# Optimization experiments

Hardware: AMD Instinct MI355X
Metric: run time of the kernel (lower is better)

## Reference

```python
import jax, jax.numpy as jnp
import numpy as np
import math

B, L, DV = 8, 2048, 512
FACTOR = 5
SAMPLE_K = min(FACTOR * int(np.ceil(np.log(L))), L)  # 40
N_TOP = min(FACTOR * int(np.ceil(np.log(L))), L)     # 40


def setup_inputs() -> dict:
    key = jax.random.key(0)
    k1, k2, k3, k4, k5 = jax.random.split(key, 5)
    x = jax.random.normal(k1, (B, L, DV), dtype=jnp.float32)
    Wq = jax.random.normal(k2, (DV, DV), dtype=jnp.float32) * (1.0 / math.sqrt(DV))
    Wk = jax.random.normal(k3, (DV, DV), dtype=jnp.float32) * (1.0 / math.sqrt(DV))
    Wv = jax.random.normal(k4, (DV, DV), dtype=jnp.float32) * (1.0 / math.sqrt(DV))
    index_sample = jax.random.randint(k5, (L, SAMPLE_K), 0, L, dtype=jnp.int32)
    return {"x": x, "Wq": Wq, "Wk": Wk, "Wv": Wv, "index_sample": index_sample}


def reference(x, Wq, Wk, Wv, index_sample):
    # Projections (torch Linear, no bias): y = x @ W.T
    Q = x @ Wq.T  # [B, L, D]
    K = x @ Wk.T  # [B, L, D]
    V = x @ Wv.T  # [B, L, D]
    b, L_Q, D = Q.shape
    L_K = K.shape[1]

    # _prob_QK: sample keys per query, score sparsity measure M
    K_sample = K[:, index_sample, :]                       # [B, L_Q, sample_k, D]
    QK_sample = jnp.einsum('bld,blsd->bls', Q, K_sample)   # [B, L_Q, sample_k]
    M = QK_sample.max(axis=-1) - QK_sample.sum(axis=-1) / L_K  # [B, L_Q]
    _, M_top = jax.lax.top_k(M, N_TOP)                     # [B, n_top]

    Q_reduce = jnp.take_along_axis(Q, M_top[:, :, None], axis=1)  # [B, n_top, D]
    scores = jnp.einsum('bud,bkd->buk', Q_reduce, K)       # [B, n_top, L_K]
    scores = scores * (1.0 / math.sqrt(D))

    # mask_flag=False -> initial context is mean of V broadcast over queries
    attn = jax.nn.softmax(scores, axis=-1)
    context = jnp.broadcast_to(V.mean(axis=1, keepdims=True), (b, L_Q, D))
    upd = attn @ V                                         # [B, n_top, D]
    context = context.at[jnp.arange(b)[:, None], M_top].set(upd)
    return context
```

## Files before the change

kernel.cpp:

```cpp
#include <hip/hip_runtime.h>
#include <hip/hip_bf16.h>
#include <hip/hip_fp16.h>
#include <math.h>

#define BATCH 8
#define LSEQ 2048
#define DIM 512
#define SK 40
#define NTOP 40

typedef __attribute__((ext_vector_type(8))) short bf16x8;
typedef __attribute__((ext_vector_type(4))) float f32x4;

__device__ inline void split1(float f, ushort& h, ushort& l) {
    __hip_bfloat16 bh = __float2bfloat16(f);
    float r = f - __bfloat162float(bh);
    __hip_bfloat16 bl = __float2bfloat16(r);
    h = *reinterpret_cast<ushort*>(&bh);
    l = *reinterpret_cast<ushort*>(&bl);
}

__global__ __launch_bounds__(256) void convert_all(
    const float* __restrict__ x,
    const float* __restrict__ w0, const float* __restrict__ w1, const float* __restrict__ w2,
    ushort* __restrict__ xh, ushort* __restrict__ xl,
    ushort* __restrict__ wh, ushort* __restrict__ wl)
{
    const int bx = blockIdx.x;
    const float* src;
    ushort *dh, *dl;
    int i;
    if (bx < 8192) {
        i = (bx * 256 + (int)threadIdx.x) * 4;
        src = x; dh = xh; dl = xl;
    } else {
        const int j = bx - 8192;
        const int z = j >> 8;
        src = (z == 0) ? w0 : (z == 1) ? w1 : w2;
        dh = wh + (size_t)z * DIM * DIM;
        dl = wl + (size_t)z * DIM * DIM;
        i = ((j & 255) * 256 + (int)threadIdx.x) * 4;
    }
    float4 v = *reinterpret_cast<const float4*>(src + i);
    ushort4 h, l;
    split1(v.x, h.x, l.x); split1(v.y, h.y, l.y);
    split1(v.z, h.z, l.z); split1(v.w, h.w, l.w);
    *reinterpret_cast<ushort4*>(dh + i) = h;
    *reinterpret_cast<ushort4*>(dl + i) = l;
}

__device__ inline void load_lds16(const void* g, void* l) {
    __builtin_amdgcn_global_load_lds(
        (const __attribute__((address_space(1))) void*)g,
        (__attribute__((address_space(3))) void*)l, 16, 0, 0);
}

__global__ __launch_bounds__(256) void gemm_mfma(
    const ushort* __restrict__ xh, const ushort* __restrict__ xl,
    const ushort* __restrict__ whAll, const ushort* __restrict__ wlAll,
    float* __restrict__ Q, float* __restrict__ K, float* __restrict__ V,
    ushort* __restrict__ Khalf)
{
    const ushort* Wh = whAll + (size_t)blockIdx.z * DIM * DIM;
    const ushort* Wl = wlAll + (size_t)blockIdx.z * DIM * DIM;
    float* C = (blockIdx.z == 0) ? Q : (blockIdx.z == 1) ? K : V;
    const bool wk = (Khalf != nullptr) && (blockIdx.z == 1);

    __shared__ ushort Ah[128 * 32], Al[128 * 32], Bh[128 * 32], Bl[128 * 32];

    const int tid  = threadIdx.x;
    const int lane = tid & 63;
    const int w    = tid >> 6;
    const int row0 = blockIdx.x * 128;
    const int col0 = blockIdx.y * 128;
    const int wr = w >> 1, wc = w & 1;

    const int rA  = w * 16 + (lane >> 2);
    const int sh_ = (lane & 3) ^ ((rA >> 1) & 3);
    const size_t aoff = (size_t)(row0 + rA) * DIM + sh_ * 8;
    const size_t boff = (size_t)(col0 + rA) * DIM + sh_ * 8;

    f32x4 acc[4][4];
    #pragma unroll
    for (int i = 0; i < 4; ++i)
        #pragma unroll
        for (int j = 0; j < 4; ++j)
            acc[i][j] = (f32x4){0.f, 0.f, 0.f, 0.f};

    const int rbA = wr * 64 + (lane & 15);
    const int rbB = wc * 64 + (lane & 15);
    const int kh  = lane >> 4;

    for (int k0 = 0; k0 < DIM; k0 += 32) {
        load_lds16(xh + aoff + k0,            &Ah[w * 512]);
        load_lds16(xh + aoff + 64 * DIM + k0, &Ah[2048 + w * 512]);
        load_lds16(xl + aoff + k0,            &Al[w * 512]);
        load_lds16(xl + aoff + 64 * DIM + k0, &Al[2048 + w * 512]);
        load_lds16(Wh + boff + k0,            &Bh[w * 512]);
        load_lds16(Wh + boff + 64 * DIM + k0, &Bh[2048 + w * 512]);
        load_lds16(Wl + boff + k0,            &Bl[w * 512]);
        load_lds16(Wl + boff + 64 * DIM + k0, &Bl[2048 + w * 512]);
        __syncthreads();

        bf16x8 fah[4], fal[4], fbh[4], fbl[4];
        #pragma unroll
        for (int mf = 0; mf < 4; ++mf) {
            const int r = rbA + mf * 16;
            const int off = r * 32 + (kh ^ ((r >> 1) & 3)) * 8;
            fah[mf] = *reinterpret_cast<const bf16x8*>(&Ah[off]);
            fal[mf] = *reinterpret_cast<const bf16x8*>(&Al[off]);
        }
        #pragma unroll
        for (int nf = 0; nf < 4; ++nf) {
            const int r = rbB + nf * 16;
            const int off = r * 32 + (kh ^ ((r >> 1) & 3)) * 8;
            fbh[nf] = *reinterpret_cast<const bf16x8*>(&Bh[off]);
            fbl[nf] = *reinterpret_cast<const bf16x8*>(&Bl[off]);
        }
        #pragma unroll
        for (int mf = 0; mf < 4; ++mf)
            #pragma unroll
            for (int nf = 0; nf < 4; ++nf) {
                acc[mf][nf] = __builtin_amdgcn_mfma_f32_16x16x32_bf16(fah[mf], fbh[nf], acc[mf][nf], 0, 0, 0);
                acc[mf][nf] = __builtin_amdgcn_mfma_f32_16x16x32_bf16(fal[mf], fbh[nf], acc[mf][nf], 0, 0, 0);
                acc[mf][nf] = __builtin_amdgcn_mfma_f32_16x16x32_bf16(fah[mf], fbl[nf], acc[mf][nf], 0, 0, 0);
            }
        __syncthreads();
    }

    #pragma unroll
    for (int mf = 0; mf < 4; ++mf)
        #pragma unroll
        for (int nf = 0; nf < 4; ++nf) {
            const size_t rbase = (size_t)(row0 + wr * 64 + mf * 16 + (lane >> 4) * 4);
            const int    cidx  = col0 + wc * 64 + nf * 16 + (lane & 15);
            float* cp = C + rbase * DIM + cidx;
            #pragma unroll
            for (int j = 0; j < 4; ++j) {
                cp[(size_t)j * DIM] = acc[mf][nf][j];
                if (wk) {
                    __half h = __float2half(acc[mf][nf][j]);
                    Khalf[(rbase + j) * DIM + cidx] = *reinterpret_cast<ushort*>(&h);
                }
            }
        }
}

#define BM 64
#define BN 64
#define BKD 32
__global__ __launch_bounds__(256) void gemm_qkv(
    const float* __restrict__ x,
    const float* __restrict__ Wq, const float* __restrict__ Wk, const float* __restrict__ Wv,
    float* __restrict__ Q, float* __restrict__ K, float* __restrict__ V)
{
    const float* W;
    float* C;
    if (blockIdx.z == 0)      { W = Wq; C = Q; }
    else if (blockIdx.z == 1) { W = Wk; C = K; }
    else                      { W = Wv; C = V; }

    __shared__ float As[BKD][BM];
    __shared__ float Bs[BKD][BN];

    const int tid  = threadIdx.x;
    const int row0 = blockIdx.x * BM;
    const int col0 = blockIdx.y * BN;
    const int ty   = tid >> 4;
    const int tx   = tid & 15;
    const int lrow = tid >> 3;
    const int lkq  = tid & 7;

    float acc[4][4] = {};
    for (int k0 = 0; k0 < DIM; k0 += BKD) {
        #pragma unroll
        for (int h = 0; h < 2; ++h) {
            const int arow = lrow + h * 32;
            float4 va = *reinterpret_cast<const float4*>(&x[(size_t)(row0 + arow) * DIM + k0 + lkq * 4]);
            As[lkq * 4 + 0][arow] = va.x; As[lkq * 4 + 1][arow] = va.y;
            As[lkq * 4 + 2][arow] = va.z; As[lkq * 4 + 3][arow] = va.w;
            float4 vb = *reinterpret_cast<const float4*>(&W[(size_t)(col0 + arow) * DIM + k0 + lkq * 4]);
            Bs[lkq * 4 + 0][arow] = vb.x; Bs[lkq * 4 + 1][arow] = vb.y;
            Bs[lkq * 4 + 2][arow] = vb.z; Bs[lkq * 4 + 3][arow] = vb.w;
        }
        __syncthreads();
        #pragma unroll
        for (int kk = 0; kk < BKD; ++kk) {
            float4 a4 = *reinterpret_cast<const float4*>(&As[kk][ty * 4]);
            float4 b4 = *reinterpret_cast<const float4*>(&Bs[kk][tx * 4]);
            float af[4] = {a4.x, a4.y, a4.z, a4.w};
            float bf[4] = {b4.x, b4.y, b4.z, b4.w};
            #pragma unroll
            for (int i = 0; i < 4; ++i)
                #pragma unroll
                for (int j = 0; j < 4; ++j)
                    acc[i][j] += af[i] * bf[j];
        }
        __syncthreads();
    }
    #pragma unroll
    for (int i = 0; i < 4; ++i) {
        float4 o = make_float4(acc[i][0], acc[i][1], acc[i][2], acc[i][3]);
        *reinterpret_cast<float4*>(&C[(size_t)(row0 + ty * 4 + i) * DIM + col0 + tx * 4]) = o;
    }
}

__global__ __launch_bounds__(512) void m_and_vp(
    const float* __restrict__ Q, const float* __restrict__ K,
    const ushort* __restrict__ Khalf,
    const float* __restrict__ V, const int* __restrict__ smp,
    float* __restrict__ M, float* __restrict__ P)
{
    const int bid = blockIdx.x;
    if (bid < 2048) {
        const int wv   = threadIdx.x >> 6;
        const int lane = threadIdx.x & 63;
        const int b    = bid & 7;
        const int l    = (bid >> 3) * 8 + wv;

        const float* qr = Q + ((size_t)b * LSEQ + l) * DIM;
        float4 q0 = *reinterpret_cast<const float4*>(&qr[lane * 8]);
        float4 q1 = *reinterpret_cast<const float4*>(&qr[lane * 8 + 4]);
        const float qf[8] = {q0.x, q0.y, q0.z, q0.w, q1.x, q1.y, q1.z, q1.w};

        const int* sp = smp + l * SK;
        float mx = -1e30f, sm = 0.0f;

        if (Khalf) {
            const ushort* Kb = Khalf + (size_t)b * LSEQ * DIM;
            for (int s = 0; s < SK; s += 8) {
                int4 i0 = *reinterpret_cast<const int4*>(sp + s);
                int4 i1 = *reinterpret_cast<const int4*>(sp + s + 4);
                const int id[8] = {i0.x, i0.y, i0.z, i0.w, i1.x, i1.y, i1.z, i1.w};
                float p[8];
                #pragma unroll
                for (int j = 0; j < 8; ++j) {
                    float4 hv = *reinterpret_cast<const float4*>(Kb + (size_t)id[j] * DIM + lane * 8);
                    const __half* h = reinterpret_cast<const __half*>(&hv);
                    float d = 0.0f;
                    #pragma unroll
                    for (int e = 0; e < 8; ++e) d = fmaf(qf[e], __half2float(h[e]), d);
                    p[j] = d;
                }
                #pragma unroll
                for (int o = 32; o; o >>= 1) {
                    #pragma unroll
                    for (int j = 0; j < 8; ++j) p[j] += __shfl_xor(p[j], o, 64);
                }
                #pragma unroll
                for (int j = 0; j < 8; ++j) { mx = fmaxf(mx, p[j]); sm += p[j]; }
            }
        } else {
            const float* Kb = K + (size_t)b * LSEQ * DIM;
            for (int s = 0; s < SK; s += 8) {
                int4 i0 = *reinterpret_cast<const int4*>(sp + s);
                int4 i1 = *reinterpret_cast<const int4*>(sp + s + 4);
                const int id[8] = {i0.x, i0.y, i0.z, i0.w, i1.x, i1.y, i1.z, i1.w};
                float p[8];
                #pragma unroll
                for (int j = 0; j < 8; ++j) {
                    const float* r = Kb + (size_t)id[j] * DIM + lane * 8;
                    float4 u0 = *reinterpret_cast<const float4*>(r);
                    float4 u1 = *reinterpret_cast<const float4*>(r + 4);
                    p[j] = q0.x*u0.x + q0.y*u0.y + q0.z*u0.z + q0.w*u0.w
                         + q1.x*u1.x + q1.y*u1.y + q1.z*u1.z + q1.w*u1.w;
                }
                #pragma unroll
                for (int o = 32; o; o >>= 1) {
                    #pragma unroll
                    for (int j = 0; j < 8; ++j) p[j] += __shfl_xor(p[j], o, 64);
                }
                #pragma unroll
                for (int j = 0; j < 8; ++j) { mx = fmaxf(mx, p[j]); sm += p[j]; }
            }
        }
        if (lane == 0) M[(size_t)b * LSEQ + l] = mx - sm * (1.0f / LSEQ);
    } else {
        const int j = bid - 2048;
        const int b = j & 7, c = j >> 3;
        const int d = threadIdx.x;
        const float* vp = V + ((size_t)b * LSEQ + c * 128) * DIM + d;
        float s = 0.0f;
        for (int r = 0; r < 128; ++r) s += vp[(size_t)r * DIM];
        P[(size_t)(b * 16 + c) * DIM + d] = s;
    }
}

__global__ __launch_bounds__(512) void refine_kernel(
    const float* __restrict__ Mc, const float* __restrict__ Q,
    const float* __restrict__ K, const int* __restrict__ smp,
    float* __restrict__ Mf)
{
    const int b   = blockIdx.x & 7;
    const int lch = blockIdx.x >> 3;
    const int wv   = threadIdx.x >> 6;
    const int lane = threadIdx.x & 63;
    __shared__ float sT0;

    if (threadIdx.x < 64) {
        float v[32];
        #pragma unroll
        for (int r = 0; r < 32; ++r) v[r] = Mc[(size_t)b * LSEQ + lane + r * 64];
        float T0 = -1e30f;
        for (int t = 0; t < 56; ++t) {
            float bv = -1e30f; int bk = 0;
            #pragma unroll
            for (int r = 0; r < 32; ++r) if (v[r] > bv) { bv = v[r]; bk = r; }
            int bl = lane;
            #pragma unroll
            for (int o = 32; o; o >>= 1) {
                float ov = __shfl_xor(bv, o, 64);
                int   obl = __shfl_xor(bl, o, 64);
                int   obk = __shfl_xor(bk, o, 64);
                if (ov > bv || (ov == bv && obl < bl)) { bv = ov; bl = obl; bk = obk; }
            }
            if (lane == bl) v[bk] = -1e30f;
            T0 = bv;
        }
        if (lane == 0) sT0 = T0;
    }
    __syncthreads();
    const float thr = sT0 - 0.25f;

    const int lbase = lch * 64 + wv * 8;
    for (int i = 0; i < 8; ++i) {
        const int l = lbase + i;
        const float cheap = Mc[(size_t)b * LSEQ + l];
        if (cheap > thr) {
            const float* qr = Q + ((size_t)b * LSEQ + l) * DIM;
            float4 q0 = *reinterpret_cast<const float4*>(&qr[lane * 8]);
            float4 q1 = *reinterpret_cast<const float4*>(&qr[lane * 8 + 4]);
            const int* sp = smp + l * SK;
            const float* Kb = K + (size_t)b * LSEQ * DIM;
            float mx = -1e30f, sm = 0.0f;
            for (int s = 0; s < SK; s += 8) {
                int4 i0 = *reinterpret_cast<const int4*>(sp + s);
                int4 i1 = *reinterpret_cast<const int4*>(sp + s + 4);
                const int id[8] = {i0.x, i0.y, i0.z, i0.w, i1.x, i1.y, i1.z, i1.w};
                float p[8];
                #pragma unroll
                for (int j = 0; j < 8; ++j) {
                    const float* r = Kb + (size_t)id[j] * DIM + lane * 8;
                    float4 u0 = *reinterpret_cast<const float4*>(r);
                    float4 u1 = *reinterpret_cast<const float4*>(r + 4);
                    p[j] = q0.x*u0.x + q0.y*u0.y + q0.z*u0.z + q0.w*u0.w
                         + q1.x*u1.x + q1.y*u1.y + q1.z*u1.z + q1.w*u1.w;
                }
                #pragma unroll
                for (int o = 32; o; o >>= 1) {
                    #pragma unroll
                    for (int j = 0; j < 8; ++j) p[j] += __shfl_xor(p[j], o, 64);
                }
                #pragma unroll
                for (int j = 0; j < 8; ++j) { mx = fmaxf(mx, p[j]); sm += p[j]; }
            }
            if (lane == 0) Mf[(size_t)b * LSEQ + l] = mx - sm * (1.0f / LSEQ);
        } else {
            if (lane == 0) Mf[(size_t)b * LSEQ + l] = cheap;
        }
    }
}

__global__ __launch_bounds__(512) void topk_vr(
    const float* __restrict__ M, const float* __restrict__ P,
    int* __restrict__ topidx, float* __restrict__ vmean)
{
    if (blockIdx.x < 8) {
        if (threadIdx.x >= 64) return;
        const int b = blockIdx.x;
        const int lane = threadIdx.x;
        float v[32];
        #pragma unroll
        for (int r = 0; r < 32; ++r) v[r] = M[(size_t)b * LSEQ + lane + r * 64];
        for (int t = 0; t < NTOP; ++t) {
            float bv = -1e30f; int bk = 0;
            #pragma unroll
            for (int r = 0; r < 32; ++r) if (v[r] > bv) { bv = v[r]; bk = r; }
            int bi = lane + bk * 64;
            #pragma unroll
            for (int o = 32; o; o >>= 1) {
                float ov = __shfl_xor(bv, o, 64);
                int   oi = __shfl_xor(bi, o, 64);
                if (ov > bv || (ov == bv && oi < bi)) { bv = ov; bi = oi; }
            }
            if (lane == (bi & 63)) v[bi >> 6] = -1e30f;
            if (lane == 0) topidx[b * NTOP + t] = bi;
        }
    } else {
        const int b = blockIdx.x - 8;
        const int d = threadIdx.x;
        float s = 0.0f;
        #pragma unroll
        for (int c = 0; c < 16; ++c) s += P[(size_t)(b * 16 + c) * DIM + d];
        vmean[b * DIM + d] = s * (1.0f / LSEQ);
    }
}

__global__ __launch_bounds__(256) void fill_out(
    const float4* __restrict__ vmean4, float4* __restrict__ out4)
{
    const int f = blockIdx.x * 256 + threadIdx.x;
    const int d4 = f & 127;
    const int b  = f >> 18;
    out4[f] = vmean4[b * 128 + d4];
}

__global__ __launch_bounds__(256) void scores_kernel(
    const float* __restrict__ Q, const float* __restrict__ K,
    const int* __restrict__ topidx, float* __restrict__ S)
{
    const int b  = blockIdx.x & 7;
    const int lc = blockIdx.x >> 3;
    __shared__ float Qs[40 * 132];
    __shared__ float Ks[64 * 132];
    __shared__ int tix[NTOP];
    const int tid = threadIdx.x;
    const int lt  = tid & 31;
    const int ug  = tid >> 5;
    float acc[2][5] = {};

    if (tid < NTOP) tix[tid] = topidx[b * NTOP + tid];
    __syncthreads();

    for (int d0 = 0; d0 < DIM; d0 += 128) {
        for (int j = tid; j < 1280; j += 256) {
            const int u = j >> 5, d4 = j & 31;
            *reinterpret_cast<float4*>(&Qs[u * 132 + d4 * 4]) =
                *reinterpret_cast<const float4*>(&Q[((size_t)b * LSEQ + tix[u]) * DIM + d0 + d4 * 4]);
        }
        for (int j = tid; j < 2048; j += 256) {
            const int l = j >> 5, d4 = j & 31;
            *reinterpret_cast<float4*>(&Ks[l * 132 + d4 * 4]) =
                *reinterpret_cast<const float4*>(&K[((size_t)b * LSEQ + lc * 64 + l) * DIM + d0 + d4 * 4]);
        }
        __syncthreads();
        for (int d4 = 0; d4 < 32; ++d4) {
            float4 ka = *reinterpret_cast<const float4*>(&Ks[lt * 132 + d4 * 4]);
            float4 kb = *reinterpret_cast<const float4*>(&Ks[(lt + 32) * 132 + d4 * 4]);
            #pragma unroll
            for (int i = 0; i < 5; ++i) {
                float4 q = *reinterpret_cast<const float4*>(&Qs[(ug + i * 8) * 132 + d4 * 4]);
                acc[0][i] += q.x * ka.x + q.y * ka.y + q.z * ka.z + q.w * ka.w;
                acc[1][i] += q.x * kb.x + q.y * kb.y + q.z * kb.z + q.w * kb.w;
            }
        }
        __syncthreads();
    }
    const float scale = 0.044194173824159216f;
    #pragma unroll
    for (int i = 0; i < 5; ++i) {
        const int u = ug + i * 8;
        S[((size_t)(b * NTOP + u)) * LSEQ + lc * 64 + lt]      = acc[0][i] * scale;
        S[((size_t)(b * NTOP + u)) * LSEQ + lc * 64 + lt + 32] = acc[1][i] * scale;
    }
}

__global__ __launch_bounds__(256) void softmax_kernel(
    const float* __restrict__ S, float* __restrict__ Pt)
{
    const int row = blockIdx.x;
    const int b = row / NTOP, u = row % NTOP;
    __shared__ float red[4];
    const int tid  = threadIdx.x;
    const int lane = tid & 63;
    const int wave = tid >> 6;
    const float* sr = S + (size_t)row * LSEQ;

    float v[8];
    float mx = -1e30f;
    #pragma unroll
    for (int j = 0; j < 8; ++j) { v[j] = sr[tid + j * 256]; mx = fmaxf(mx, v[j]); }
    #pragma unroll
    for (int o = 32; o; o >>= 1) mx = fmaxf(mx, __shfl_xor(mx, o, 64));
    if (lane == 0) red[wave] = mx;
    __syncthreads();
    mx = fmaxf(fmaxf(red[0], red[1]), fmaxf(red[2], red[3]));
    __syncthreads();

    float s = 0.0f;
    #pragma unroll
    for (int j = 0; j < 8; ++j) { v[j] = __expf(v[j] - mx); s += v[j]; }
    #pragma unroll
    for (int o = 32; o; o >>= 1) s += __shfl_xor(s, o, 64);
    if (lane == 0) red[wave] = s;
    __syncthreads();
    const float rec = 1.0f / (red[0] + red[1] + red[2] + red[3]);

    #pragma unroll
    for (int j = 0; j < 8; ++j)
        Pt[((size_t)b * LSEQ + tid + j * 256) * NTOP + u] = v[j] * rec;
}

__global__ __launch_bounds__(512) void pv_partial(
    const float* __restrict__ Pt, const float* __restrict__ V, float* __restrict__ Ppart)
{
    const int b  = blockIdx.x & 7;
    const int lc = blockIdx.x >> 3;
    const int d  = threadIdx.x;
    float part[NTOP] = {};
    for (int lg = 0; lg < 32; ++lg) {
        const int l = lc * 128 + lg * 4;
        const float v0 = V[((size_t)b * LSEQ + l + 0) * DIM + d];
        const float v1 = V[((size_t)b * LSEQ + l + 1) * DIM + d];
        const float v2 = V[((size_t)b * LSEQ + l + 2) * DIM + d];
        const float v3 = V[((size_t)b * LSEQ + l + 3) * DIM + d];
        const float4* p0 = reinterpret_cast<const float4*>(Pt + ((size_t)b * LSEQ + l + 0) * NTOP);
        const float4* p1 = reinterpret_cast<const float4*>(Pt + ((size_t)b * LSEQ + l + 1) * NTOP);
        const float4* p2 = reinterpret_cast<const float4*>(Pt + ((size_t)b * LSEQ + l + 2) * NTOP);
        const float4* p3 = reinterpret_cast<const float4*>(Pt + ((size_t)b * LSEQ + l + 3) * NTOP);
        #pragma unroll
        for (int u4 = 0; u4 < 10; ++u4) {
            float4 a = p0[u4], bb = p1[u4], c = p2[u4], dd = p3[u4];
            part[u4*4+0] = fmaf(a.x, v0, fmaf(bb.x, v1, fmaf(c.x, v2, fmaf(dd.x, v3, part[u4*4+0]))));
            part[u4*4+1] = fmaf(a.y, v0, fmaf(bb.y, v1, fmaf(c.y, v2, fmaf(dd.y, v3, part[u4*4+1]))));
            part[u4*4+2] = fmaf(a.z, v0, fmaf(bb.z, v1, fmaf(c.z, v2, fmaf(dd.z, v3, part[u4*4+2]))));
            part[u4*4+3] = fmaf(a.w, v0, fmaf(bb.w, v1, fmaf(c.w, v2, fmaf(dd.w, v3, part[u4*4+3]))));
        }
    }
    #pragma unroll
    for (int u = 0; u < NTOP; ++u)
        Ppart[(((size_t)(b * 16 + lc)) * NTOP + u) * DIM + d] = part[u];
}

__global__ __launch_bounds__(512) void pv_reduce(
    const float* __restrict__ Ppart, const int* __restrict__ topidx, float* __restrict__ out)
{
    const int row = blockIdx.x;
    const int b = row / NTOP, u = row % NTOP;
    const int d = threadIdx.x;
    float s = 0.0f;
    #pragma unroll
    for (int lc = 0; lc < 16; ++lc)
        s += Ppart[(((size_t)(b * 16 + lc)) * NTOP + u) * DIM + d];
    out[((size_t)b * LSEQ + topidx[row]) * DIM + d] = s;
}

__global__ __launch_bounds__(256) void att_kernel(
    const float* __restrict__ Q, const float* __restrict__ K, const float* __restrict__ V,
    const int* __restrict__ topidx, float* __restrict__ out)
{
    const int b = blockIdx.x / NTOP;
    const int u = blockIdx.x % NTOP;
    const int l0 = topidx[b * NTOP + u];

    __shared__ float p[LSEQ];
    __shared__ float redm[4];
    __shared__ float reds[4];

    const int tid  = threadIdx.x;
    const int lane = tid & 63;
    const int wave = tid >> 6;

    const float* qr = Q + ((size_t)b * LSEQ + l0) * DIM;
    float4 q0 = *reinterpret_cast<const float4*>(&qr[lane * 8]);
    float4 q1 = *reinterpret_cast<const float4*>(&qr[lane * 8 + 4]);
    const float scale = 0.044194173824159216f;

    for (int it = 0; it < 512; ++it) {
        const int l = wave * 512 + it;
        const float* kr = K + ((size_t)b * LSEQ + l) * DIM;
        float4 k0 = *reinterpret_cast<const float4*>(&kr[lane * 8]);
        float4 k1 = *reinterpret_cast<const float4*>(&kr[lane * 8 + 4]);
        float d = q0.x * k0.x + q0.y * k0.y + q0.z * k0.z + q0.w * k0.w
                + q1.x * k1.x + q1.y * k1.y + q1.z * k1.z + q1.w * k1.w;
        #pragma unroll
        for (int o = 32; o; o >>= 1) d += __shfl_xor(d, o, 64);
        if (lane == 0) p[l] = d * scale;
    }
    __syncthreads();

    float mx = -1e30f;
    for (int i = tid; i < LSEQ; i += 256) mx = fmaxf(mx, p[i]);
    #pragma unroll
    for (int o = 32; o; o >>= 1) mx = fmaxf(mx, __shfl_xor(mx, o, 64));
    if (lane == 0) redm[wave] = mx;
    __syncthreads();
    mx = fmaxf(fmaxf(redm[0], redm[1]), fmaxf(redm[2], redm[3]));

    float s = 0.0f;
    for (int i = tid; i < LSEQ; i += 256) {
        float e = __expf(p[i] - mx);
        s += e;
        p[i] = e;
    }
    #pragma unroll
    for (int o = 32; o; o >>= 1) s += __shfl_xor(s, o, 64);
    if (lane == 0) reds[wave] = s;
    __syncthreads();
    const float rec = 1.0f / (reds[0] + reds[1] + reds[2] + reds[3]);

    float s0 = 0.0f, s1 = 0.0f;
    const float* vp = V + (size_t)b * LSEQ * DIM;
    for (int l = 0; l < LSEQ; ++l) {
        const float w = p[l];
        s0 += w * vp[(size_t)l * DIM + tid];
        s1 += w * vp[(size_t)l * DIM + tid + 256];
    }
    float* orow = out + ((size_t)b * LSEQ + l0) * DIM;
    orow[tid]       = s0 * rec;
    orow[tid + 256] = s1 * rec;
}

extern "C" void kernel_launch(void* const* d_in, const int* in_sizes, int n_in,
                              void* d_out, int out_size, void* d_ws, size_t ws_size,
                              hipStream_t stream)
{
    const float* x   = (const float*)d_in[0];
    const float* Wq  = (const float*)d_in[1];
    const float* Wk  = (const float*)d_in[2];
    const float* Wv  = (const float*)d_in[3];
    const int*   smp = (const int*)d_in[4];
    float* out = (float*)d_out;

    const size_t NQKV = (size_t)BATCH * LSEQ * DIM;
    float* ws = (float*)d_ws;

    float* Q     = ws;
    float* K     = Q + NQKV;
    float* V     = K + NQKV;
    float* Mb    = V + NQKV;
    float* vmP   = Mb + BATCH * LSEQ;
    float* vmean = vmP + BATCH * 16 * DIM;
    float* S     = vmean + BATCH * DIM;
    float* Pt    = S + (size_t)BATCH * NTOP * LSEQ;
    float* Mf    = Pt + (size_t)BATCH * NTOP * LSEQ;
    float* Ppart = Mf + (size_t)BATCH * LSEQ;
    int*   topidx = (int*)(Ppart + (size_t)BATCH * 16 * NTOP * DIM);
    ushort* xh = (ushort*)(topidx + BATCH * NTOP);
    ushort* xl = xh + NQKV;
    ushort* wh = xl + NQKV;
    ushort* wl = wh + (size_t)3 * DIM * DIM;
    ushort* Khalf = wl + (size_t)3 * DIM * DIM;
    const size_t need_fast2 = (size_t)((char*)(Khalf + NQKV) - (char*)d_ws);
    const size_t need_fast  = (size_t)((char*)Khalf - (char*)d_ws);
    const size_t need_mid   = (size_t)((char*)(topidx + BATCH * NTOP) - (char*)d_ws);

    const bool fast2 = ws_size >= need_fast2;
    const bool fast  = ws_size >= need_fast;
    const bool mid   = ws_size >= need_mid;

    if (mid) {
        ushort* kh = nullptr;
        if (fast) {
            kh = fast2 ? Khalf : nullptr;
            convert_all<<<8960, 256, 0, stream>>>(x, Wq, Wk, Wv, xh, xl, wh, wl);
            gemm_mfma<<<dim3(BATCH * LSEQ / 128, DIM / 128, 3), 256, 0, stream>>>(
                xh, xl, wh, wl, Q, K, V, kh);
        } else {
            gemm_qkv<<<dim3(BATCH * LSEQ / BM, DIM / BN, 3), 256, 0, stream>>>(
                x, Wq, Wk, Wv, Q, K, V);
        }
        m_and_vp<<<2176, 512, 0, stream>>>(Q, K, kh, V, smp, Mb, vmP);
        const float* Msel = Mb;
        if (kh) {
            refine_kernel<<<256, 512, 0, stream>>>(Mb, Q, K, smp, Mf);
            Msel = Mf;
        }
        topk_vr<<<16, 512, 0, stream>>>(Msel, vmP, topidx, vmean);
        fill_out<<<(BATCH * LSEQ * DIM / 4) / 256, 256, 0, stream>>>(
            (const float4*)vmean, (float4*)out);
        scores_kernel<<<256, 256, 0, stream>>>(Q, K, topidx, S);
        softmax_kernel<<<BATCH * NTOP, 256, 0, stream>>>(S, Pt);
        pv_partial<<<128, 512, 0, stream>>>(Pt, V, Ppart);
        pv_reduce<<<BATCH * NTOP, 512, 0, stream>>>(Ppart, topidx, out);
    } else {
        float* Qf = ws;
        float* Kf = Qf + NQKV;
        float* Vf = Kf + NQKV;
        float* Mfb = Vf + NQKV;
        int*   ti = (int*)(Mfb + (size_t)BATCH * LSEQ);
        float* Pf = (float*)(ti + BATCH * NTOP);
        float* vm = Pf + (size_t)BATCH * 16 * DIM;

        gemm_qkv<<<dim3(BATCH * LSEQ / BM, DIM / BN, 3), 256, 0, stream>>>(
            x, Wq, Wk, Wv, Qf, Kf, Vf);
        m_and_vp<<<2176, 512, 0, stream>>>(Qf, Kf, nullptr, Vf, smp, Mfb, Pf);
        topk_vr<<<16, 512, 0, stream>>>(Mfb, Pf, ti, vm);
        fill_out<<<(BATCH * LSEQ * DIM / 4) / 256, 256, 0, stream>>>(
            (const float4*)vm, (float4*)out);
        att_kernel<<<BATCH * NTOP, 256, 0, stream>>>(Qf, Kf, Vf, ti, out);
    }
}
```

Baseline: 373.7 us.

## Fuse candidate refinement into top-k kernel and move fp16 K conversion to own kernel

```diff
diff --git a/kernel.cpp b/kernel.cpp
--- a/kernel.cpp
+++ b/kernel.cpp
@@ -8,8 +8,10 @@
 #define DIM 512
 #define SK 40
 #define NTOP 40
+#define NCAND 56
 
 typedef __attribute__((ext_vector_type(8))) short bf16x8;
+typedef __attribute__((ext_vector_type(8))) ushort u16x8;
 typedef __attribute__((ext_vector_type(4))) float f32x4;
 
 __device__ inline void split1(float f, ushort& h, ushort& l) {
@@ -58,13 +60,11 @@
 __global__ __launch_bounds__(256) void gemm_mfma(
     const ushort* __restrict__ xh, const ushort* __restrict__ xl,
     const ushort* __restrict__ whAll, const ushort* __restrict__ wlAll,
-    float* __restrict__ Q, float* __restrict__ K, float* __restrict__ V,
-    ushort* __restrict__ Khalf)
+    float* __restrict__ Q, float* __restrict__ K, float* __restrict__ V)
 {
     const ushort* Wh = whAll + (size_t)blockIdx.z * DIM * DIM;
     const ushort* Wl = wlAll + (size_t)blockIdx.z * DIM * DIM;
     float* C = (blockIdx.z == 0) ? Q : (blockIdx.z == 1) ? K : V;
-    const bool wk = (Khalf != nullptr) && (blockIdx.z == 1);
 
     __shared__ ushort Ah[128 * 32], Al[128 * 32], Bh[128 * 32], Bl[128 * 32];
 
@@ -132,18 +132,28 @@
     for (int mf = 0; mf < 4; ++mf)
         #pragma unroll
         for (int nf = 0; nf < 4; ++nf) {
-            const size_t rbase = (size_t)(row0 + wr * 64 + mf * 16 + (lane >> 4) * 4);
-            const int    cidx  = col0 + wc * 64 + nf * 16 + (lane & 15);
-            float* cp = C + rbase * DIM + cidx;
-            #pragma unroll
-            for (int j = 0; j < 4; ++j) {
+            float* cp = C + (size_t)(row0 + wr * 64 + mf * 16 + (lane >> 4) * 4) * DIM
+                          + col0 + wc * 64 + nf * 16 + (lane & 15);
+            #pragma unroll
+            for (int j = 0; j < 4; ++j)
                 cp[(size_t)j * DIM] = acc[mf][nf][j];
-                if (wk) {
-                    __half h = __float2half(acc[mf][nf][j]);
-                    Khalf[(rbase + j) * DIM + cidx] = *reinterpret_cast<ushort*>(&h);
-                }
-            }
-        }
+        }
+}
+
+__global__ __launch_bounds__(256) void k2half(
+    const float* __restrict__ K, ushort* __restrict__ Kh)
+{
+    const int i = (blockIdx.x * 256 + (int)threadIdx.x) * 8;
+    float4 a = *reinterpret_cast<const float4*>(K + i);
+    float4 b = *reinterpret_cast<const float4*>(K + i + 4);
+    const float f[8] = {a.x, a.y, a.z, a.w, b.x, b.y, b.z, b.w};
+    u16x8 r;
+    #pragma unroll
+    for (int e = 0; e < 8; ++e) {
+        __half h = __float2half(f[e]);
+        r[e] = *reinterpret_cast<ushort*>(&h);
+    }
+    *reinterpret_cast<u16x8*>(Kh + i) = r;
 }
 
 #define BM 64
@@ -286,113 +296,107 @@
     }
 }
 
-__global__ __launch_bounds__(512) void refine_kernel(
-    const float* __restrict__ Mc, const float* __restrict__ Q,
-    const float* __restrict__ K, const int* __restrict__ smp,
-    float* __restrict__ Mf)
-{
-    const int b   = blockIdx.x & 7;
-    const int lch = blockIdx.x >> 3;
-    const int wv   = threadIdx.x >> 6;
-    const int lane = threadIdx.x & 63;
-    __shared__ float sT0;
-
-    if (threadIdx.x < 64) {
-        float v[32];
-        #pragma unroll
-        for (int r = 0; r < 32; ++r) v[r] = Mc[(size_t)b * LSEQ + lane + r * 64];
-        float T0 = -1e30f;
-        for (int t = 0; t < 56; ++t) {
-            float bv = -1e30f; int bk = 0;
-            #pragma unroll
-            for (int r = 0; r < 32; ++r) if (v[r] > bv) { bv = v[r]; bk = r; }
-            int bl = lane;
-            #pragma unroll
-            for (int o = 32; o; o >>= 1) {
-                float ov = __shfl_xor(bv, o, 64);
-                int   obl = __shfl_xor(bl, o, 64);
-                int   obk = __shfl_xor(bk, o, 64);
-                if (ov > bv || (ov == bv && obl < bl)) { bv = ov; bl = obl; bk = obk; }
-            }
-            if (lane == bl) v[bk] = -1e30f;
-            T0 = bv;
-        }
-        if (lane == 0) sT0 = T0;
-    }
-    __syncthreads();
-    const float thr = sT0 - 0.25f;
-
-    const int lbase = lch * 64 + wv * 8;
-    for (int i = 0; i < 8; ++i) {
-        const int l = lbase + i;
-        const float cheap = Mc[(size_t)b * LSEQ + l];
-        if (cheap > thr) {
-            const float* qr = Q + ((size_t)b * LSEQ + l) * DIM;
-            float4 q0 = *reinterpret_cast<const float4*>(&qr[lane * 8]);
-            float4 q1 = *reinterpret_cast<const float4*>(&qr[lane * 8 + 4]);
-            const int* sp = smp + l * SK;
-            const float* Kb = K + (size_t)b * LSEQ * DIM;
-            float mx = -1e30f, sm = 0.0f;
-            for (int s = 0; s < SK; s += 8) {
-                int4 i0 = *reinterpret_cast<const int4*>(sp + s);
-                int4 i1 = *reinterpret_cast<const int4*>(sp + s + 4);
-                const int id[8] = {i0.x, i0.y, i0.z, i0.w, i1.x, i1.y, i1.z, i1.w};
-                float p[8];
-                #pragma unroll
-                for (int j = 0; j < 8; ++j) {
-                    const float* r = Kb + (size_t)id[j] * DIM + lane * 8;
-                    float4 u0 = *reinterpret_cast<const float4*>(r);
-                    float4 u1 = *reinterpret_cast<const float4*>(r + 4);
-                    p[j] = q0.x*u0.x + q0.y*u0.y + q0.z*u0.z + q0.w*u0.w
-                         + q1.x*u1.x + q1.y*u1.y + q1.z*u1.z + q1.w*u1.w;
-                }
-                #pragma unroll
-                for (int o = 32; o; o >>= 1) {
-                    #pragma unroll
-                    for (int j = 0; j < 8; ++j) p[j] += __shfl_xor(p[j], o, 64);
-                }
-                #pragma unroll
-                for (int j = 0; j < 8; ++j) { mx = fmaxf(mx, p[j]); sm += p[j]; }
-            }
-            if (lane == 0) Mf[(size_t)b * LSEQ + l] = mx - sm * (1.0f / LSEQ);
-        } else {
-            if (lane == 0) Mf[(size_t)b * LSEQ + l] = cheap;
-        }
-    }
-}
-
 __global__ __launch_bounds__(512) void topk_vr(
     const float* __restrict__ M, const float* __restrict__ P,
+    const float* __restrict__ Q, const float* __restrict__ K,
+    const int* __restrict__ smp, const int refine,
     int* __restrict__ topidx, float* __restrict__ vmean)
 {
-    if (blockIdx.x < 8) {
-        if (threadIdx.x >= 64) return;
-        const int b = blockIdx.x;
-        const int lane = threadIdx.x;
+    if (blockIdx.x >= 8) {
+        const int b = blockIdx.x - 8;
+        const int d = threadIdx.x;
+        float s = 0.0f;
+        #pragma unroll
+        for (int c = 0; c < 16; ++c) s += P[(size_t)(b * 16 + c) * DIM + d];
+        vmean[b * DIM + d] = s * (1.0f / LSEQ);
+        return;
+    }
+
+    const int b    = blockIdx.x;
+    const int tid  = threadIdx.x;
+    const int lane = tid & 63;
+    const int wv   = tid >> 6;
+
+    __shared__ int   cidx[NCAND];
+    __shared__ float cval[NCAND];
+
+    if (tid < 64) {
         float v[32];
         #pragma unroll
-        for (int r = 0; r < 32; ++r) v[r] = M[(size_t)b * LSEQ + lane + r * 64];
-        for (int t = 0; t < NTOP; ++t) {
-            float bv = -1e30f; int bk = 0;
-            #pragma unroll
-            for (int r = 0; r < 32; ++r) if (v[r] > bv) { bv = v[r]; bk = r; }
-            int bi = lane + bk * 64;
+        for (int r = 0; r < 32; ++r) v[r] = M[(size_t)b * LSEQ + lane + (r << 6)];
+        const int rounds = refine ? NCAND : NTOP;
+        for (int t = 0; t < rounds; ++t) {
+            float bv = -1e30f; int bi = 0x7fffffff;
+            #pragma unroll
+            for (int r = 0; r < 32; ++r) {
+                const int ii = lane + (r << 6);
+                if (v[r] > bv) { bv = v[r]; bi = ii; }
+            }
             #pragma unroll
             for (int o = 32; o; o >>= 1) {
                 float ov = __shfl_xor(bv, o, 64);
                 int   oi = __shfl_xor(bi, o, 64);
                 if (ov > bv || (ov == bv && oi < bi)) { bv = ov; bi = oi; }
             }
-            if (lane == (bi & 63)) v[bi >> 6] = -1e30f;
+            #pragma unroll
+            for (int r = 0; r < 32; ++r)
+                v[r] = (lane + (r << 6) == bi) ? -1e30f : v[r];
+            if (lane == 0) {
+                if (refine) { cidx[t] = bi; cval[t] = bv; }
+                else        topidx[b * NTOP + t] = bi;
+            }
+        }
+    }
+    if (!refine) return;
+    __syncthreads();
+
+    for (int j = wv; j < NCAND; j += 8) {
+        const int l = cidx[j];
+        const float* qr = Q + ((size_t)b * LSEQ + l) * DIM;
+        float4 q0 = *reinterpret_cast<const float4*>(&qr[lane * 8]);
+        float4 q1 = *reinterpret_cast<const float4*>(&qr[lane * 8 + 4]);
+        const int* sp = smp + l * SK;
+        const float* Kb = K + (size_t)b * LSEQ * DIM;
+        float mx = -1e30f, sm = 0.0f;
+        for (int s = 0; s < SK; s += 8) {
+            int4 i0 = *reinterpret_cast<const int4*>(sp + s);
+            int4 i1 = *reinterpret_cast<const int4*>(sp + s + 4);
+            const int id[8] = {i0.x, i0.y, i0.z, i0.w, i1.x, i1.y, i1.z, i1.w};
+            float p[8];
+            #pragma unroll
+            for (int jj = 0; jj < 8; ++jj) {
+                const float* r = Kb + (size_t)id[jj] * DIM + lane * 8;
+                float4 u0 = *reinterpret_cast<const float4*>(r);
+                float4 u1 = *reinterpret_cast<const float4*>(r + 4);
+                p[jj] = q0.x*u0.x + q0.y*u0.y + q0.z*u0.z + q0.w*u0.w
+                      + q1.x*u1.x + q1.y*u1.y + q1.z*u1.z + q1.w*u1.w;
+            }
+            #pragma unroll
+            for (int o = 32; o; o >>= 1) {
+                #pragma unroll
+                for (int jj = 0; jj < 8; ++jj) p[jj] += __shfl_xor(p[jj], o, 64);
+            }
+            #pragma unroll
+            for (int jj = 0; jj < 8; ++jj) { mx = fmaxf(mx, p[jj]); sm += p[jj]; }
+        }
+        if (lane == 0) cval[j] = mx - sm * (1.0f / LSEQ);
+    }
+    __syncthreads();
+
+    if (tid < 64) {
+        float mv = (lane < NCAND) ? cval[lane] : -1e30f;
+        int   mi = (lane < NCAND) ? cidx[lane] : 0x7fffffff;
+        for (int t = 0; t < NTOP; ++t) {
+            float bv = mv; int bi = mi;
+            #pragma unroll
+            for (int o = 32; o; o >>= 1) {
+                float ov = __shfl_xor(bv, o, 64);
+                int   oi = __shfl_xor(bi, o, 64);
+                if (ov > bv || (ov == bv && oi < bi)) { bv = ov; bi = oi; }
+            }
             if (lane == 0) topidx[b * NTOP + t] = bi;
-        }
-    } else {
-        const int b = blockIdx.x - 8;
-        const int d = threadIdx.x;
-        float s = 0.0f;
-        #pragma unroll
-        for (int c = 0; c < 16; ++c) s += P[(size_t)(b * 16 + c) * DIM + d];
-        vmean[b * DIM + d] = s * (1.0f / LSEQ);
+            if (mi == bi) mv = -1e30f;
+        }
     }
 }
 
@@ -623,8 +627,8 @@
     float* vmean = vmP + BATCH * 16 * DIM;
     float* S     = vmean + BATCH * DIM;
     float* Pt    = S + (size_t)BATCH * NTOP * LSEQ;
-    float* Mf    = Pt + (size_t)BATCH * NTOP * LSEQ;
-    float* Ppart = Mf + (size_t)BATCH * LSEQ;
+    float* Qsel  = Pt + (size_t)BATCH * NTOP * LSEQ;
+    float* Ppart = Qsel + (size_t)BATCH * NTOP * DIM;
     int*   topidx = (int*)(Ppart + (size_t)BATCH * 16 * NTOP * DIM);
     ushort* xh = (ushort*)(topidx + BATCH * NTOP);
     ushort* xl = xh + NQKV;
@@ -642,21 +646,19 @@
     if (mid) {
         ushort* kh = nullptr;
         if (fast) {
-            kh = fast2 ? Khalf : nullptr;
             convert_all<<<8960, 256, 0, stream>>>(x, Wq, Wk, Wv, xh, xl, wh, wl);
             gemm_mfma<<<dim3(BATCH * LSEQ / 128, DIM / 128, 3), 256, 0, stream>>>(
-                xh, xl, wh, wl, Q, K, V, kh);
+                xh, xl, wh, wl, Q, K, V);
+            if (fast2) {
+                kh = Khalf;
+                k2half<<<NQKV / 2048, 256, 0, stream>>>(K, Khalf);
+            }
         } else {
             gemm_qkv<<<dim3(BATCH * LSEQ / BM, DIM / BN, 3), 256, 0, stream>>>(
                 x, Wq, Wk, Wv, Q, K, V);
         }
         m_and_vp<<<2176, 512, 0, stream>>>(Q, K, kh, V, smp, Mb, vmP);
-        const float* Msel = Mb;
-        if (kh) {
-            refine_kernel<<<256, 512, 0, stream>>>(Mb, Q, K, smp, Mf);
-            Msel = Mf;
-        }
-        topk_vr<<<16, 512, 0, stream>>>(Msel, vmP, topidx, vmean);
+        topk_vr<<<16, 512, 0, stream>>>(Mb, vmP, Q, K, smp, kh ? 1 : 0, topidx, vmean);
         fill_out<<<(BATCH * LSEQ * DIM / 4) / 256, 256, 0, stream>>>(
             (const float4*)vmean, (float4*)out);
         scores_kernel<<<256, 256, 0, stream>>>(Q, K, topidx, S);
@@ -667,15 +669,15 @@
         float* Qf = ws;
         float* Kf = Qf + NQKV;
         float* Vf = Kf + NQKV;
-        float* Mfb = Vf + NQKV;
-        int*   ti = (int*)(Mfb + (size_t)BATCH * LSEQ);
+        float* Mf = Vf + NQKV;
+        int*   ti = (int*)(Mf + (size_t)BATCH * LSEQ);
         float* Pf = (float*)(ti + BATCH * NTOP);
         float* vm = Pf + (size_t)BATCH * 16 * DIM;
 
         gemm_qkv<<<dim3(BATCH * LSEQ / BM, DIM / BN, 3), 256, 0, stream>>>(
             x, Wq, Wk, Wv, Qf, Kf, Vf);
-        m_and_vp<<<2176, 512, 0, stream>>>(Qf, Kf, nullptr, Vf, smp, Mfb, Pf);
-        topk_vr<<<16, 512, 0, stream>>>(Mfb, Pf, ti, vm);
+        m_and_vp<<<2176, 512, 0, stream>>>(Qf, Kf, nullptr, Vf, smp, Mf, Pf);
+        topk_vr<<<16, 512, 0, stream>>>(Mf, Pf, Qf, Kf, smp, 0, ti, vm);
         fill_out<<<(BATCH * LSEQ * DIM / 4) / 256, 256, 0, stream>>>(
             (const float4*)vm, (float4*)out);
         att_kernel<<<BATCH * NTOP, 256, 0, stream>>>(Qf, Kf, Vf, ti, out);
```

Result: slower. 404.2 us (+8.2%).

## Move fp16 K conversion to a separate vectorized kernel and parallelize top-k

Applied to the files above, without the earlier changes.

```diff
diff --git a/kernel.cpp b/kernel.cpp
--- a/kernel.cpp
+++ b/kernel.cpp
@@ -10,6 +10,7 @@
 #define NTOP 40
 
 typedef __attribute__((ext_vector_type(8))) short bf16x8;
+typedef __attribute__((ext_vector_type(8))) ushort u16x8;
 typedef __attribute__((ext_vector_type(4))) float f32x4;
 
 __device__ inline void split1(float f, ushort& h, ushort& l) {
@@ -58,13 +59,11 @@
 __global__ __launch_bounds__(256) void gemm_mfma(
     const ushort* __restrict__ xh, const ushort* __restrict__ xl,
     const ushort* __restrict__ whAll, const ushort* __restrict__ wlAll,
-    float* __restrict__ Q, float* __restrict__ K, float* __restrict__ V,
-    ushort* __restrict__ Khalf)
+    float* __restrict__ Q, float* __restrict__ K, float* __restrict__ V)
 {
     const ushort* Wh = whAll + (size_t)blockIdx.z * DIM * DIM;
     const ushort* Wl = wlAll + (size_t)blockIdx.z * DIM * DIM;
     float* C = (blockIdx.z == 0) ? Q : (blockIdx.z == 1) ? K : V;
-    const bool wk = (Khalf != nullptr) && (blockIdx.z == 1);
 
     __shared__ ushort Ah[128 * 32], Al[128 * 32], Bh[128 * 32], Bl[128 * 32];
 
@@ -132,18 +131,28 @@
     for (int mf = 0; mf < 4; ++mf)
         #pragma unroll
         for (int nf = 0; nf < 4; ++nf) {
-            const size_t rbase = (size_t)(row0 + wr * 64 + mf * 16 + (lane >> 4) * 4);
-            const int    cidx  = col0 + wc * 64 + nf * 16 + (lane & 15);
-            float* cp = C + rbase * DIM + cidx;
-            #pragma unroll
-            for (int j = 0; j < 4; ++j) {
+            float* cp = C + (size_t)(row0 + wr * 64 + mf * 16 + (lane >> 4) * 4) * DIM
+                          + col0 + wc * 64 + nf * 16 + (lane & 15);
+            #pragma unroll
+            for (int j = 0; j < 4; ++j)
                 cp[(size_t)j * DIM] = acc[mf][nf][j];
-                if (wk) {
-                    __half h = __float2half(acc[mf][nf][j]);
-                    Khalf[(rbase + j) * DIM + cidx] = *reinterpret_cast<ushort*>(&h);
-                }
-            }
-        }
+        }
+}
+
+__global__ __launch_bounds__(256) void k2half(
+    const float* __restrict__ K, ushort* __restrict__ Kh)
+{
+    const int i = (blockIdx.x * 256 + (int)threadIdx.x) * 8;
+    float4 a = *reinterpret_cast<const float4*>(K + i);
+    float4 b = *reinterpret_cast<const float4*>(K + i + 4);
+    const float f[8] = {a.x, a.y, a.z, a.w, b.x, b.y, b.z, b.w};
+    u16x8 r;
+    #pragma unroll
+    for (int e = 0; e < 8; ++e) {
+        __half h = __float2half(f[e]);
+        r[e] = *reinterpret_cast<ushort*>(&h);
+    }
+    *reinterpret_cast<u16x8*>(Kh + i) = r;
 }
 
 #define BM 64
@@ -291,8 +300,8 @@
     const float* __restrict__ K, const int* __restrict__ smp,
     float* __restrict__ Mf)
 {
-    const int b   = blockIdx.x & 7;
-    const int lch = blockIdx.x >> 3;
+    const int b    = blockIdx.x & 7;
+    const int lch  = blockIdx.x >> 3;
     const int wv   = threadIdx.x >> 6;
     const int lane = threadIdx.x & 63;
     __shared__ float sT0;
@@ -300,21 +309,24 @@
     if (threadIdx.x < 64) {
         float v[32];
         #pragma unroll
-        for (int r = 0; r < 32; ++r) v[r] = Mc[(size_t)b * LSEQ + lane + r * 64];
+        for (int r = 0; r < 32; ++r) v[r] = Mc[(size_t)b * LSEQ + lane + (r << 6)];
         float T0 = -1e30f;
         for (int t = 0; t < 56; ++t) {
-            float bv = -1e30f; int bk = 0;
-            #pragma unroll
-            for (int r = 0; r < 32; ++r) if (v[r] > bv) { bv = v[r]; bk = r; }
-            int bl = lane;
+            float bv = -1e30f; int bi = 0x7fffffff;
+            #pragma unroll
+            for (int r = 0; r < 32; ++r) {
+                const int ii = lane + (r << 6);
+                if (v[r] > bv) { bv = v[r]; bi = ii; }
+            }
             #pragma unroll
             for (int o = 32; o; o >>= 1) {
                 float ov = __shfl_xor(bv, o, 64);
-                int   obl = __shfl_xor(bl, o, 64);
-                int   obk = __shfl_xor(bk, o, 64);
-                if (ov > bv || (ov == bv && obl < bl)) { bv = ov; bl = obl; bk = obk; }
-            }
-            if (lane == bl) v[bk] = -1e30f;
+                int   oi = __shfl_xor(bi, o, 64);
+                if (ov > bv || (ov == bv && oi < bi)) { bv = ov; bi = oi; }
+            }
+            #pragma unroll
+            for (int r = 0; r < 32; ++r)
+                v[r] = (lane + (r << 6) == bi) ? -1e30f : v[r];
             T0 = bv;
         }
         if (lane == 0) sT0 = T0;
@@ -365,26 +377,52 @@
     const float* __restrict__ M, const float* __restrict__ P,
     int* __restrict__ topidx, float* __restrict__ vmean)
 {
+    __shared__ float vals[LSEQ];
+    __shared__ float wvv[8];
+    __shared__ int   wii[8];
+
     if (blockIdx.x < 8) {
-        if (threadIdx.x >= 64) return;
         const int b = blockIdx.x;
-        const int lane = threadIdx.x;
-        float v[32];
-        #pragma unroll
-        for (int r = 0; r < 32; ++r) v[r] = M[(size_t)b * LSEQ + lane + r * 64];
+        const int tid  = threadIdx.x;
+        const int lane = tid & 63;
+        const int wave = tid >> 6;
+
+        #pragma unroll
+        for (int q = 0; q < 4; ++q) vals[tid + q * 512] = M[b * LSEQ + tid + q * 512];
+        __syncthreads();
+
         for (int t = 0; t < NTOP; ++t) {
-            float bv = -1e30f; int bk = 0;
-            #pragma unroll
-            for (int r = 0; r < 32; ++r) if (v[r] > bv) { bv = v[r]; bk = r; }
-            int bi = lane + bk * 64;
+            float bv = -1e30f;
+            int   bi = 0x7fffffff;
+            #pragma unroll
+            for (int q = 0; q < 4; ++q) {
+                const int ii = tid + q * 512;
+                const float v = vals[ii];
+                if (v > bv) { bv = v; bi = ii; }
+            }
             #pragma unroll
             for (int o = 32; o; o >>= 1) {
                 float ov = __shfl_xor(bv, o, 64);
                 int   oi = __shfl_xor(bi, o, 64);
                 if (ov > bv || (ov == bv && oi < bi)) { bv = ov; bi = oi; }
             }
-            if (lane == (bi & 63)) v[bi >> 6] = -1e30f;
-            if (lane == 0) topidx[b * NTOP + t] = bi;
+            if (lane == 0) { wvv[wave] = bv; wii[wave] = bi; }
+            __syncthreads();
+            if (wave == 0) {
+                float fv = (lane < 8) ? wvv[lane] : -1e30f;
+                int   fi = (lane < 8) ? wii[lane] : 0x7fffffff;
+                #pragma unroll
+                for (int o = 4; o; o >>= 1) {
+                    float ov = __shfl_xor(fv, o, 64);
+                    int   oi = __shfl_xor(fi, o, 64);
+                    if (ov > fv || (ov == fv && oi < fi)) { fv = ov; fi = oi; }
+                }
+                if (lane == 0) {
+                    topidx[b * NTOP + t] = fi;
+                    vals[fi] = -1e30f;
+                }
+            }
+            __syncthreads();
         }
     } else {
         const int b = blockIdx.x - 8;
@@ -624,7 +662,7 @@
     float* S     = vmean + BATCH * DIM;
     float* Pt    = S + (size_t)BATCH * NTOP * LSEQ;
     float* Mf    = Pt + (size_t)BATCH * NTOP * LSEQ;
-    float* Ppart = Mf + (size_t)BATCH * LSEQ;
+    float* Ppart = Mf + (size_t)BATCH * NTOP * DIM;
     int*   topidx = (int*)(Ppart + (size_t)BATCH * 16 * NTOP * DIM);
     ushort* xh = (ushort*)(topidx + BATCH * NTOP);
     ushort* xl = xh + NQKV;
@@ -642,10 +680,13 @@
     if (mid) {
         ushort* kh = nullptr;
         if (fast) {
-            kh = fast2 ? Khalf : nullptr;
             convert_all<<<8960, 256, 0, stream>>>(x, Wq, Wk, Wv, xh, xl, wh, wl);
             gemm_mfma<<<dim3(BATCH * LSEQ / 128, DIM / 128, 3), 256, 0, stream>>>(
-                xh, xl, wh, wl, Q, K, V, kh);
+                xh, xl, wh, wl, Q, K, V);
+            if (fast2) {
+                kh = Khalf;
+                k2half<<<NQKV / 2048, 256, 0, stream>>>(K, Khalf);
+            }
         } else {
             gemm_qkv<<<dim3(BATCH * LSEQ / BM, DIM / BN, 3), 256, 0, stream>>>(
                 x, Wq, Wk, Wv, Q, K, V);
```

Measured after the change: 373.8 us. No clear change (+0.0%).
